# Kernel tuning notes

Hardware: AMD Instinct MI355X
Metric: run time of the kernel (lower is better)

## Reference

```python
import jax, jax.numpy as jnp
import numpy as np


def _conv(x, w, b, pad):
    y = jax.lax.conv_general_dilated(
        x, w, window_strides=(1, 1), padding=[(pad, pad), (pad, pad)],
        dimension_numbers=('NCHW', 'OIHW', 'NCHW'))
    return y + b[None, :, None, None]


def _grid_sample(img, gxn, gyn):
    # img [N,C,H,W]; gxn,gyn [N,H,W] normalized coords.
    # Matches torch grid_sample(mode='bilinear', padding_mode='zeros', align_corners=False).
    N, C, H, W = img.shape
    ix = ((gxn + 1.0) * W - 1.0) * 0.5
    iy = ((gyn + 1.0) * H - 1.0) * 0.5
    ix0 = jnp.floor(ix); iy0 = jnp.floor(iy)
    ix1 = ix0 + 1.0; iy1 = iy0 + 1.0
    wx1 = ix - ix0; wy1 = iy - iy0
    wx0 = 1.0 - wx1; wy0 = 1.0 - wy1
    bidx = jnp.arange(N)[:, None, None]

    def gather(yy, xx):
        valid = (xx >= 0) & (xx < W) & (yy >= 0) & (yy < H)
        xc = jnp.clip(xx, 0, W - 1).astype(jnp.int32)
        yc = jnp.clip(yy, 0, H - 1).astype(jnp.int32)
        v = img[bidx, :, yc, xc]  # [N,H,W,C]
        return jnp.where(valid[..., None], v, jnp.zeros((), img.dtype))

    out = (gather(iy0, ix0) * (wy0 * wx0)[..., None]
           + gather(iy0, ix1) * (wy0 * wx1)[..., None]
           + gather(iy1, ix0) * (wy1 * wx0)[..., None]
           + gather(iy1, ix1) * (wy1 * wx1)[..., None])
    return jnp.transpose(out, (0, 3, 1, 2))  # [N,C,H,W]


def reference(inputs, state, i2h_w, i2h_b, i2f_w, i2f_b, h2f_w, h2f_b,
              flows_w, flows_b, wrap_w, wrap_b):
    B, T, Cin, H, W = inputs.shape
    hid = state.shape[1]
    L = flows_w.shape[0] // 2

    # input-to-hidden for all timesteps at once (as in the torch code)
    i2h = _conv(inputs.reshape(B * T, Cin, H, W), i2h_w, i2h_b, 1)
    i2h = i2h.reshape(B, T, 3 * hid, H, W)
    r_i, u_i, n_i = jnp.split(i2h, 3, axis=2)

    gx, gy = jnp.meshgrid(jnp.arange(W, dtype=inputs.dtype),
                          jnp.arange(H, dtype=inputs.dtype))  # each [H,W]

    def step(h, xs):
        x_t, r_t, u_t, n_t = xs
        f = jnp.tanh(_conv(x_t, i2f_w, i2f_b, 2) + _conv(h, h2f_w, h2f_b, 2))
        flows = _conv(f, flows_w, flows_b, 2).reshape(B, L, 2, H, W)
        # vgrid = grid + (-flow), then normalize by 2*v/size - 1
        vx = gx[None, None] - flows[:, :, 0]
        vy = gy[None, None] - flows[:, :, 1]
        gxn = 2.0 * vx / W - 1.0
        gyn = 2.0 * vy / H - 1.0
        img = jnp.broadcast_to(h[:, None], (B, L, hid, H, W)).reshape(B * L, hid, H, W)
        warped = _grid_sample(img, gxn.reshape(B * L, H, W), gyn.reshape(B * L, H, W))
        warped = warped.reshape(B, L * hid, H, W)
        h2h = _conv(warped, wrap_w, wrap_b, 0)
        r_h, u_h, n_h = jnp.split(h2h, 3, axis=1)
        r = jax.nn.sigmoid(r_t + r_h)
        u = jax.nn.sigmoid(u_t + u_h)
        n = jax.nn.sigmoid(n_t + r * n_h)  # note: sigmoid, faithful to source
        h_new = (1.0 - u) * n + u * h
        return h_new, h_new

    xs = (jnp.swapaxes(inputs, 0, 1),
          jnp.swapaxes(r_i, 0, 1),
          jnp.swapaxes(u_i, 0, 1),
          jnp.swapaxes(n_i, 0, 1))
    h_last, outs = jax.lax.scan(step, state, xs)
    outputs = jnp.swapaxes(outs, 0, 1)  # [B,T,hid,H,W]
    return outputs, h_last


def setup_inputs() -> dict:
    key = jax.random.key(0)
    ks = jax.random.split(key, 8)
    B, T, Cin, H, W = 4, 10, 8, 96, 96
    hid, L = 64, 13

    def w(k, shape):
        fan_in = int(np.prod(shape[1:]))
        return jax.random.normal(k, shape, jnp.float32) * (1.0 / np.sqrt(fan_in))

    return {
        'inputs': jax.random.normal(ks[0], (B, T, Cin, H, W), jnp.float32),
        'state': jnp.zeros((B, hid, H, W), jnp.float32),
        'i2h_w': w(ks[1], (3 * hid, Cin, 3, 3)), 'i2h_b': jnp.zeros((3 * hid,), jnp.float32),
        'i2f_w': w(ks[2], (32, Cin, 5, 5)), 'i2f_b': jnp.zeros((32,), jnp.float32),
        'h2f_w': w(ks[3], (32, hid, 5, 5)), 'h2f_b': jnp.zeros((32,), jnp.float32),
        'flows_w': w(ks[4], (2 * L, 32, 5, 5)), 'flows_b': jnp.zeros((2 * L,), jnp.float32),
        'wrap_w': w(ks[5], (3 * hid, hid * L, 1, 1)), 'wrap_b': jnp.zeros((3 * hid,), jnp.float32),
    }
```

## Files before the change

kernel.cpp:

```cpp
#include <hip/hip_runtime.h>
#include <math.h>

#define HW 9216

typedef __attribute__((ext_vector_type(8))) short short8;
typedef __attribute__((ext_vector_type(4))) short short4v;
typedef __attribute__((ext_vector_type(4))) float float4v;

__device__ __forceinline__ float sigmoidf_(float x) { return 1.0f / (1.0f + expf(-x)); }

__device__ __forceinline__ short bf16rne(float f) {
  unsigned u = __builtin_bit_cast(unsigned, f);
  unsigned r = (u + 0x7FFFu + ((u >> 16) & 1u)) >> 16;
  return (short)r;
}
__device__ __forceinline__ float bf2f(short s) {
  return __builtin_bit_cast(float, ((unsigned)(unsigned short)s) << 16);
}

__global__ __launch_bounds__(256) void k_wconv(const float* __restrict__ w,
                                               short* __restrict__ o)
{
  int i = blockIdx.x * 256 + threadIdx.x;
  if (i >= 192 * 832) return;
  int n = i / 832, k = i % 832;
  int l = k >> 6, c = k & 63;
  o[((size_t)l * 192 + n) * 64 + c] = bf16rne(w[i]);
}

__global__ __launch_bounds__(256) void k_pack(
    const float* __restrict__ wh, const float* __restrict__ wi,
    const float* __restrict__ flw, const float* __restrict__ wih,
    short* __restrict__ whK, short* __restrict__ wiK, short* __restrict__ flK,
    short* __restrict__ i2hK)
{
  int i = blockIdx.x * 256 + threadIdx.x;
  if (i < 51200) {
    int t = i / 2048, rem = i % 2048;
    int o = rem / 64, c = rem % 64;
    whK[i] = bf16rne(wh[((size_t)(o * 64 + c)) * 25 + t]);
  } else if (i < 58368) {
    int j = i - 51200;
    int g = j / 1024, rem = j % 1024;
    int o = rem / 32, k = rem % 32;
    int q = k / 8, ch = k % 8;
    int tap = g * 4 + q;
    wiK[j] = (tap < 25) ? bf16rne(wi[((size_t)(o * 8 + ch)) * 25 + tap]) : (short)0;
  } else if (i < 83968) {
    int j = i - 58368;
    int t = j / 1024, rem = j % 1024;
    int o = rem / 32, c = rem % 32;
    flK[j] = (o < 26) ? bf16rne(flw[((size_t)(o * 32 + c)) * 25 + t]) : (short)0;
  } else {
    int j = i - 83968;
    int g = j / 6144, rem = j % 6144;
    int n = rem / 32, k = rem % 32;
    int q = k / 8, ch = k % 8;
    int tap = g * 4 + q;
    i2hK[j] = (tap < 9) ? bf16rne(wih[((size_t)(n * 8 + ch)) * 9 + tap]) : (short)0;
  }
}

__global__ __launch_bounds__(256) void k_h2bf(const float* __restrict__ st,
                                              short* __restrict__ hbf)
{
  const int tid = threadIdx.x;
  const int pp = tid & 63, cg = tid >> 6;
  const int b = blockIdx.y;
  const int p = blockIdx.x * 64 + pp;
  short s[16];
  #pragma unroll
  for (int k = 0; k < 16; ++k)
    s[k] = bf16rne(st[((size_t)b * 64 + cg * 16 + k) * HW + p]);
  short* dst = hbf + ((size_t)b * HW + p) * 64 + cg * 16;
  *(short8*)dst = *(short8*)&s[0];
  *(short8*)(dst + 8) = *(short8*)&s[8];
}

__global__ __launch_bounds__(256) void k_x2bf(const float* __restrict__ inp,
                                              short* __restrict__ xbf)
{
  const int p  = blockIdx.x * 256 + threadIdx.x;
  const int bt = blockIdx.y;
  short s[8];
  #pragma unroll
  for (int ci = 0; ci < 8; ++ci)
    s[ci] = bf16rne(inp[((size_t)bt * 8 + ci) * HW + p]);
  *(short8*)(xbf + ((size_t)bt * HW + p) * 8) = *(short8*)s;
}

__global__ __launch_bounds__(256) void k_i2h(
    const short* __restrict__ xbf, int t_off,
    const short* __restrict__ wK, const float* __restrict__ bias,
    short* __restrict__ out)
{
  __shared__ __align__(16) short lds_o[192 * 136];
  const int tid  = threadIdx.x;
  const int lane = tid & 63;
  const int w    = tid >> 6;
  const int ml = lane & 15, qd = lane >> 4;
  const int zz = blockIdx.y;
  const int t = (zz >> 2) + t_off, b = zz & 3;
  const int pw0 = blockIdx.x * 128 + w * 32;
  const short* xb = xbf + ((size_t)(b * 10 + t)) * HW * 8;

  short8 afr[2][3];
  #pragma unroll
  for (int s = 0; s < 2; ++s) {
    int px0 = pw0 + s * 16;
    int y0 = px0 / 96, xc0 = px0 % 96;
    #pragma unroll
    for (int g = 0; g < 3; ++g) {
      int tap = g * 4 + qd;
      int dy = tap / 3 - 1;
      int dx = tap % 3 - 1;
      int yy = y0 + dy, xx = xc0 + ml + dx;
      bool v = (tap < 9) && (yy >= 0) && (yy < 96) && (xx >= 0) && (xx < 96);
      short8 a = {};
      if (v) a = *(const short8*)(xb + (size_t)(px0 + ml + dy * 96 + dx) * 8);
      afr[s][g] = a;
    }
  }

  float4v acc[2][12];
  #pragma unroll
  for (int s = 0; s < 2; ++s)
    #pragma unroll
    for (int j = 0; j < 12; ++j)
      #pragma unroll
      for (int r = 0; r < 4; ++r) acc[s][j][r] = 0.0f;

  #pragma unroll
  for (int j = 0; j < 12; ++j) {
    #pragma unroll
    for (int g = 0; g < 3; ++g) {
      short8 bf = *(const short8*)(wK + ((size_t)(g * 192 + j * 16 + ml)) * 32 + qd * 8);
      acc[0][j] = __builtin_amdgcn_mfma_f32_16x16x32_bf16(afr[0][g], bf, acc[0][j], 0, 0, 0);
      acc[1][j] = __builtin_amdgcn_mfma_f32_16x16x32_bf16(afr[1][g], bf, acc[1][j], 0, 0, 0);
    }
  }

  #pragma unroll
  for (int j = 0; j < 12; ++j) {
    float bv = bias[j * 16 + ml];
    #pragma unroll
    for (int s = 0; s < 2; ++s) {
      short4v o4;
      #pragma unroll
      for (int r = 0; r < 4; ++r) o4[r] = bf16rne(acc[s][j][r] + bv);
      *(short4v*)(lds_o + (j * 16 + ml) * 136 + w * 32 + s * 16 + qd * 4) = o4;
    }
  }
  __syncthreads();
  const int pblk = blockIdx.x * 128;
  #pragma unroll
  for (int k = 0; k < 12; ++k) {
    int r = (tid >> 4) + k * 16;
    short8 vvv = *(short8*)(lds_o + r * 136 + (tid & 15) * 8);
    *(short8*)(out + ((size_t)(zz * 192 + r)) * HW + pblk + (tid & 15) * 8) = vvv;
  }
}

__global__ __launch_bounds__(256) void k_f(
    const short* __restrict__ xbf, int t,
    const short* __restrict__ hbf,
    const short* __restrict__ whK,
    const short* __restrict__ wiK,
    const float* __restrict__ bi, const float* __restrict__ bh,
    short* __restrict__ fbf)
{
  const int tid = threadIdx.x;
  const int lane = tid & 63;
  const int w = tid >> 6;
  const int ml = lane & 15, qd = lane >> 4;
  const int b = blockIdx.y;
  const int px0 = blockIdx.x * 64 + w * 16;
  const int y0 = px0 / 96, xc0 = px0 % 96;
  const int xcol = xc0 + ml;
  const int px = px0 + ml;
  const short* hb = hbf + (size_t)b * HW * 64;
  const short* xb = xbf + ((size_t)(b * 10 + t)) * HW * 8;

  float4v acc0 = {0.f, 0.f, 0.f, 0.f};
  float4v acc1 = {0.f, 0.f, 0.f, 0.f};

  #pragma unroll
  for (int ky = 0; ky < 5; ++ky) {
    int yy = y0 + ky - 2;
    if (yy < 0 || yy >= 96) continue;
    #pragma unroll
    for (int kx = 0; kx < 5; ++kx) {
      int xx = xcol + kx - 2;
      bool cv = (xx >= 0) && (xx < 96);
      int off = (ky - 2) * 96 + (kx - 2);
      const short* ap = hb + (size_t)(px + off) * 64 + qd * 8;
      short8 a0 = {}, a1 = {};
      if (cv) { a0 = *(const short8*)ap; a1 = *(const short8*)(ap + 32); }
      int tap = ky * 5 + kx;
      const short* bp = whK + ((size_t)tap * 32 + ml) * 64 + qd * 8;
      short8 b00 = *(const short8*)bp;
      short8 b01 = *(const short8*)(bp + 32);
      short8 b10 = *(const short8*)(bp + 16 * 64);
      short8 b11 = *(const short8*)(bp + 16 * 64 + 32);
      acc0 = __builtin_amdgcn_mfma_f32_16x16x32_bf16(a0, b00, acc0, 0, 0, 0);
      acc0 = __builtin_amdgcn_mfma_f32_16x16x32_bf16(a1, b01, acc0, 0, 0, 0);
      acc1 = __builtin_amdgcn_mfma_f32_16x16x32_bf16(a0, b10, acc1, 0, 0, 0);
      acc1 = __builtin_amdgcn_mfma_f32_16x16x32_bf16(a1, b11, acc1, 0, 0, 0);
    }
  }

  #pragma unroll
  for (int g = 0; g < 7; ++g) {
    int tap = g * 4 + qd;
    int dy = tap / 5 - 2;
    int dx = tap - (dy + 2) * 5 - 2;
    int yy = y0 + dy, xx = xcol + dx;
    bool v = (tap < 25) && (yy >= 0) && (yy < 96) && (xx >= 0) && (xx < 96);
    short8 a = {};
    if (v) a = *(const short8*)(xb + (size_t)(px + dy * 96 + dx) * 8);
    const short* bp = wiK + ((size_t)g * 32 + ml) * 32 + qd * 8;
    short8 b0 = *(const short8*)bp;
    short8 b1 = *(const short8*)(bp + 16 * 32);
    acc0 = __builtin_amdgcn_mfma_f32_16x16x32_bf16(a, b0, acc0, 0, 0, 0);
    acc1 = __builtin_amdgcn_mfma_f32_16x16x32_bf16(a, b1, acc1, 0, 0, 0);
  }

  short* fo = fbf + (size_t)b * HW * 32;
  #pragma unroll
  for (int i = 0; i < 2; ++i) {
    int o = i * 16 + ml;
    float bias = bi[o] + bh[o];
    float4v a = i ? acc1 : acc0;
    #pragma unroll
    for (int r = 0; r < 4; ++r) {
      int p2 = px0 + qd * 4 + r;
      fo[(size_t)p2 * 32 + o] = bf16rne(tanhf(a[r] + bias));
    }
  }
}

__global__ __launch_bounds__(256) void k_flows(
    const short* __restrict__ fbf,
    const short* __restrict__ flK,
    const float* __restrict__ bias,
    float* __restrict__ fls)
{
  const int tid = threadIdx.x;
  const int lane = tid & 63;
  const int w = tid >> 6;
  const int ml = lane & 15, qd = lane >> 4;
  const int b = blockIdx.y;
  const int px0 = blockIdx.x * 64 + w * 16;
  const int y0 = px0 / 96, xc0 = px0 % 96;
  const int xcol = xc0 + ml;
  const int px = px0 + ml;
  const short* fb = fbf + (size_t)b * HW * 32;

  float4v acc0 = {0.f, 0.f, 0.f, 0.f};
  float4v acc1 = {0.f, 0.f, 0.f, 0.f};

  #pragma unroll
  for (int ky = 0; ky < 5; ++ky) {
    int yy = y0 + ky - 2;
    if (yy < 0 || yy >= 96) continue;
    #pragma unroll
    for (int kx = 0; kx < 5; ++kx) {
      int xx = xcol + kx - 2;
      bool cv = (xx >= 0) && (xx < 96);
      int off = (ky - 2) * 96 + (kx - 2);
      short8 a = {};
      if (cv) a = *(const short8*)(fb + (size_t)(px + off) * 32 + qd * 8);
      int tap = ky * 5 + kx;
      const short* bp = flK + ((size_t)tap * 32 + ml) * 32 + qd * 8;
      short8 b0 = *(const short8*)bp;
      short8 b1 = *(const short8*)(bp + 16 * 32);
      acc0 = __builtin_amdgcn_mfma_f32_16x16x32_bf16(a, b0, acc0, 0, 0, 0);
      acc1 = __builtin_amdgcn_mfma_f32_16x16x32_bf16(a, b1, acc1, 0, 0, 0);
    }
  }

  float* fo = fls + (size_t)b * 26 * HW;
  #pragma unroll
  for (int i = 0; i < 2; ++i) {
    int o = i * 16 + ml;
    if (o < 26) {
      float bv = bias[o];
      float4v a = i ? acc1 : acc0;
      #pragma unroll
      for (int r = 0; r < 4; ++r)
        fo[(size_t)o * HW + px0 + qd * 4 + r] = a[r] + bv;
    }
  }
}

__global__ __launch_bounds__(256, 3) void k_fused(
    const float* __restrict__ fls,
    const float* __restrict__ hbase, long long hstr,
    const short* __restrict__ hbf_in,
    const short* __restrict__ i2h,
    const short* __restrict__ wbf,
    const float* __restrict__ wb,
    float* __restrict__ outb, long long ostr,
    short* __restrict__ hbf_out,
    float* __restrict__ lastb)
{
  __shared__ __align__(16) char smem_raw[50176];
  short* lds_v0 = (short*)smem_raw;
  short* lds_v1 = lds_v0 + 64 * 72;
  float* lds_f  = (float*)(smem_raw + 18432);
  float* lds_h  = (float*)smem_raw;
  short* hpack  = (short*)smem_raw;

  const int tid = threadIdx.x;
  const int pp  = tid & 63;
  const int cg  = tid >> 6;
  const int ii  = blockIdx.x;
  const int xcd = ii & 7;
  const int b   = xcd >> 1;
  const int tile = ((ii >> 3) << 1) | (xcd & 1);
  const int p   = tile * 64 + pp;
  const float* hb  = hbase + (size_t)b * hstr;
  const float* flb = fls + (size_t)b * 26 * HW;
  const int ml = pp & 15;
  const int qd = pp >> 4;
  const int px_g = cg * 16 + ml;
  const int p_g  = tile * 64 + px_g;
  const int ypix = p_g / 96, xpix = p_g % 96;
  const short* hvp = hbf_in + ((size_t)b * HW) * 64 + qd * 16;
  const short* wfb = wbf + ((size_t)(48 * cg + ml)) * 64 + qd * 8;

  #pragma unroll
  for (int it = 0; it < 7; ++it) {
    int idx = it * 256 + tid;
    if (idx < 1664) {
      int c = idx >> 6, pp2 = idx & 63;
      lds_f[pp2 * 26 + c] = flb[(size_t)c * HW + tile * 64 + pp2];
    }
  }

  float4v acc[3][4];
  #pragma unroll
  for (int i = 0; i < 3; ++i)
    #pragma unroll
    for (int j = 0; j < 4; ++j)
      #pragma unroll
      for (int r = 0; r < 4; ++r) acc[i][j][r] = 0.0f;

  int   o_[4];
  float wt_[4];
  short8 u_[4][2];
  short8 wp[3][2];
  short vv[16];

  auto comp_offs = [&](int l) {
    float fx = lds_f[px_g * 26 + 2 * l];
    float fy = lds_f[px_g * 26 + 2 * l + 1];
    float ix = (float)xpix - fx - 0.5f;
    float iy = (float)ypix - fy - 0.5f;
    float x0f = floorf(ix), y0f = floorf(iy);
    float wx1 = ix - x0f, wy1 = iy - y0f;
    float wx0 = 1.0f - wx1, wy0 = 1.0f - wy1;
    int x0 = (int)x0f, y0 = (int)y0f;
    bool vx0 = (x0 >= 0) && (x0 < 96);
    bool vx1 = (x0 + 1 >= 0) && (x0 + 1 < 96);
    bool vy0g = (y0 >= 0) && (y0 < 96);
    bool vy1g = (y0 + 1 >= 0) && (y0 + 1 < 96);
    o_[0] = (vx0 && vy0g) ? (y0 * 96 + x0)           : -1;
    o_[1] = (vx1 && vy0g) ? (y0 * 96 + x0 + 1)       : -1;
    o_[2] = (vx0 && vy1g) ? ((y0 + 1) * 96 + x0)     : -1;
    o_[3] = (vx1 && vy1g) ? ((y0 + 1) * 96 + x0 + 1) : -1;
    wt_[0] = wy0 * wx0; wt_[1] = wy0 * wx1; wt_[2] = wy1 * wx0; wt_[3] = wy1 * wx1;
  };
  auto load_gather = [&]() {
    #pragma unroll
    for (int q = 0; q < 4; ++q) {
      short8 z = {};
      u_[q][0] = z; u_[q][1] = z;
      if (o_[q] >= 0) {
        const short* tp = hvp + (size_t)o_[q] * 64;
        u_[q][0] = *(const short8*)tp;
        u_[q][1] = *(const short8*)(tp + 8);
      }
    }
  };
  auto load_w = [&](int l) {
    const short* wsrc = wfb + (size_t)l * 192 * 64;
    #pragma unroll
    for (int i = 0; i < 3; ++i) {
      wp[i][0] = *(const short8*)(wsrc + (i * 16) * 64);
      wp[i][1] = *(const short8*)(wsrc + (i * 16) * 64 + 32);
    }
  };
  auto comp_vv = [&]() {
    float sum[16];
    #pragma unroll
    for (int k = 0; k < 16; ++k) sum[k] = 0.0f;
    #pragma unroll
    for (int q = 0; q < 4; ++q) {
      #pragma unroll
      for (int k = 0; k < 8; ++k) {
        sum[k]     += wt_[q] * bf2f(u_[q][0][k]);
        sum[k + 8] += wt_[q] * bf2f(u_[q][1][k]);
      }
    }
    #pragma unroll
    for (int k = 0; k < 16; ++k) vv[k] = bf16rne(sum[k]);
  };
  auto store_vv = [&](short* buf) {
    *(short8*)(buf + px_g * 72 + qd * 16)     = *(short8*)&vv[0];
    *(short8*)(buf + px_g * 72 + qd * 16 + 8) = *(short8*)&vv[8];
  };

  __syncthreads();
  comp_offs(0);
  load_gather();
  load_w(0);
  comp_vv();
  store_vv(lds_v0);

  for (int l = 0; l < 13; ++l) {
    __syncthreads();
    if (l < 12) {
      comp_offs(l + 1);
      load_gather();
    }
    short* rbuf = (l & 1) ? lds_v1 : lds_v0;
    #pragma unroll
    for (int ks = 0; ks < 2; ++ks) {
      short8 bfr[4];
      #pragma unroll
      for (int j = 0; j < 4; ++j)
        bfr[j] = *(const short8*)(rbuf + (j * 16 + ml) * 72 + ks * 32 + qd * 8);
      #pragma unroll
      for (int i = 0; i < 3; ++i)
        #pragma unroll
        for (int j = 0; j < 4; ++j)
          acc[i][j] = __builtin_amdgcn_mfma_f32_16x16x32_bf16(wp[i][ks], bfr[j], acc[i][j], 0, 0, 0);
    }
    if (l < 12) {
      load_w(l + 1);
      comp_vv();
      store_vv((l & 1) ? lds_v0 : lds_v1);
    }
  }

  __syncthreads();
  #pragma unroll
  for (int i = 0; i < 3; ++i)
    #pragma unroll
    for (int j = 0; j < 4; ++j)
      #pragma unroll
      for (int r = 0; r < 4; ++r) {
        int ch = 48 * cg + i * 16 + qd * 4 + r;
        int px = j * 16 + ml;
        lds_h[ch * 65 + px] = acc[i][j][r];
      }
  __syncthreads();

  const short* i2hb = i2h + (size_t)b * 192 * HW + p;
  float* ob = outb + (size_t)b * ostr;
  float hnv[16];
  #pragma unroll
  for (int k = 0; k < 16; ++k) {
    int cch = cg + k * 4;
    float rh = lds_h[cch * 65 + pp] + wb[cch];
    float uh = lds_h[(64 + cch) * 65 + pp] + wb[64 + cch];
    float nh = lds_h[(128 + cch) * 65 + pp] + wb[128 + cch];
    float rt = bf2f(i2hb[(size_t)cch * HW]);
    float ut = bf2f(i2hb[(size_t)(64 + cch) * HW]);
    float nt = bf2f(i2hb[(size_t)(128 + cch) * HW]);
    float rr = sigmoidf_(rt + rh);
    float uu = sigmoidf_(ut + uh);
    float nn = sigmoidf_(nt + rr * nh);
    float hp = hb[(size_t)cch * HW + p];
    float hn = (1.0f - uu) * nn + uu * hp;
    ob[(size_t)cch * HW + p] = hn;
    if (lastb) lastb[((size_t)b * 64 + cch) * HW + p] = hn;
    hnv[k] = hn;
  }

  __syncthreads();
  #pragma unroll
  for (int k = 0; k < 16; ++k)
    hpack[pp * 80 + cg + 4 * k] = bf16rne(hnv[k]);
  __syncthreads();
  {
    int px = tid >> 2, g = tid & 3;
    short8 a0 = *(short8*)(hpack + px * 80 + g * 16);
    short8 a1 = *(short8*)(hpack + px * 80 + g * 16 + 8);
    short* dst = hbf_out + ((size_t)b * HW + tile * 64 + px) * 64 + g * 16;
    *(short8*)dst = a0;
    *(short8*)(dst + 8) = a1;
  }
}

extern "C" void kernel_launch(void* const* d_in, const int* in_sizes, int n_in,
                              void* d_out, int out_size, void* d_ws, size_t ws_size,
                              hipStream_t stream)
{
  const float* inp   = (const float*)d_in[0];
  const float* state = (const float*)d_in[1];
  const float* i2h_w = (const float*)d_in[2];
  const float* i2h_b = (const float*)d_in[3];
  const float* i2f_w = (const float*)d_in[4];
  const float* i2f_b = (const float*)d_in[5];
  const float* h2f_w = (const float*)d_in[6];
  const float* h2f_b = (const float*)d_in[7];
  const float* fl_w  = (const float*)d_in[8];
  const float* fl_b  = (const float*)d_in[9];
  const float* wr_w  = (const float*)d_in[10];
  const float* wr_b  = (const float*)d_in[11];
  float* out = (float*)d_out;
  float* ws  = (float*)d_ws;

  const long long F_I2HB1 = 3538944;
  const long long F_FBF   = 589824;
  const long long F_FLS   = 958464;
  const long long F_HB    = 1179648;
  const long long F_XBF   = 1474560;
  const long long F_WBF   = 79872;
  const long long F_WHK   = 25600;
  const long long F_WIK   = 3584;
  const long long F_FLK   = 12800;
  const long long F_I2HK  = 9216;
  const long long OB      = (long long)10 * 64 * HW;

  const long long fixed = F_FBF + F_FLS + 2 * F_HB + F_XBF + F_WBF
                        + F_WHK + F_WIK + F_FLK + F_I2HK;
  bool batched = ws_size >= (size_t)(10 * F_I2HB1 + fixed) * 4ULL;
  long long i2h_fl = batched ? 10 * F_I2HB1 : F_I2HB1;

  short* ws_i2h = (short*)ws;
  float* fwp    = ws + i2h_fl;
  float* ws_fbf_f = fwp;              fwp += F_FBF;
  float* ws_fls   = fwp;              fwp += F_FLS;
  float* hbfA_f   = fwp;              fwp += F_HB;
  float* hbfB_f   = fwp;              fwp += F_HB;
  float* xbf_f    = fwp;              fwp += F_XBF;
  float* wbf_f    = fwp;              fwp += F_WBF;
  float* whK_f    = fwp;              fwp += F_WHK;
  float* wiK_f    = fwp;              fwp += F_WIK;
  float* flK_f    = fwp;              fwp += F_FLK;
  float* i2hK_f   = fwp;
  short* ws_fbf  = (short*)ws_fbf_f;
  short* hbfA    = (short*)hbfA_f;
  short* hbfB    = (short*)hbfB_f;
  short* ws_xbf  = (short*)xbf_f;
  short* ws_wbf  = (short*)wbf_f;
  short* ws_whK  = (short*)whK_f;
  short* ws_wiK  = (short*)wiK_f;
  short* ws_flK  = (short*)flK_f;
  short* ws_i2hK = (short*)i2hK_f;

  k_wconv<<<dim3(624), 256, 0, stream>>>(wr_w, ws_wbf);
  k_pack<<<dim3(400), 256, 0, stream>>>(h2f_w, i2f_w, fl_w, i2h_w,
                                        ws_whK, ws_wiK, ws_flK, ws_i2hK);
  k_h2bf<<<dim3(144, 4), 256, 0, stream>>>(state, hbfA);
  k_x2bf<<<dim3(36, 40), 256, 0, stream>>>(inp, ws_xbf);
  if (batched)
    k_i2h<<<dim3(72, 40), 256, 0, stream>>>(ws_xbf, 0, ws_i2hK, i2h_b, ws_i2h);

  for (int t = 0; t < 10; ++t) {
    const float* hbase = (t == 0) ? state : (out + (size_t)(t - 1) * 64 * HW);
    long long hstr = (t == 0) ? (long long)64 * HW : OB;
    short* hin  = (t & 1) ? hbfB : hbfA;
    short* hout = (t & 1) ? hbfA : hbfB;

    if (!batched)
      k_i2h<<<dim3(72, 4), 256, 0, stream>>>(ws_xbf, t, ws_i2hK, i2h_b, ws_i2h);
    k_f<<<dim3(144, 4), 256, 0, stream>>>(ws_xbf, t, hin, ws_whK, ws_wiK,
                                          i2f_b, h2f_b, ws_fbf);
    k_flows<<<dim3(144, 4), 256, 0, stream>>>(ws_fbf, ws_flK, fl_b, ws_fls);

    const short* i2h_t = batched ? (ws_i2h + (size_t)t * 2 * F_I2HB1) : ws_i2h;
    float* outbase = out + (size_t)t * 64 * HW;
    float* lastb = (t == 9) ? (out + (size_t)4 * 10 * 64 * HW) : nullptr;
    k_fused<<<dim3(576), 256, 0, stream>>>(ws_fls, hbase, hstr, hin, i2h_t,
                                           ws_wbf, wr_b, outbase, OB, hout, lastb);
  }
}
```

Before: 1.612 ms.

## Give each wave its own pixel slice to drop per-layer barriers in wrap MFMA

Changes the MFMA work split in the fused warp/wrap kernel. Before, each wave computed 48 output channels across all 64 pixels, which needed a shared double-buffered LDS tile and a barrier every flow layer. Now each wave computes all 192 channels for its own 16 pixels, which it gathers itself, so the per-layer __syncthreads and the second LDS buffer go away. In exchange, each wave loads the full weight slice from global/L2 every layer (4x more weight traffic), and the weight loads are no longer prefetched a layer ahead.

```diff
diff --git a/kernel.cpp b/kernel.cpp
--- a/kernel.cpp
+++ b/kernel.cpp
@@ -305,11 +305,10 @@
     float* __restrict__ lastb)
 {
   __shared__ __align__(16) char smem_raw[50176];
-  short* lds_v0 = (short*)smem_raw;
-  short* lds_v1 = lds_v0 + 64 * 72;
-  float* lds_f  = (float*)(smem_raw + 18432);
-  float* lds_h  = (float*)smem_raw;
-  short* hpack  = (short*)smem_raw;
+  short* lds_v = (short*)smem_raw;
+  float* lds_f = (float*)(smem_raw + 9216);
+  float* lds_h = (float*)smem_raw;
+  short* hpack = (short*)smem_raw;
 
   const int tid = threadIdx.x;
   const int pp  = tid & 63;
@@ -323,11 +322,10 @@
   const float* flb = fls + (size_t)b * 26 * HW;
   const int ml = pp & 15;
   const int qd = pp >> 4;
-  const int px_g = cg * 16 + ml;
-  const int p_g  = tile * 64 + px_g;
+  const int px_w = cg * 16 + ml;
+  const int p_g  = tile * 64 + px_w;
   const int ypix = p_g / 96, xpix = p_g % 96;
   const short* hvp = hbf_in + ((size_t)b * HW) * 64 + qd * 16;
-  const short* wfb = wbf + ((size_t)(48 * cg + ml)) * 64 + qd * 8;
 
   #pragma unroll
   for (int it = 0; it < 7; ++it) {
@@ -338,23 +336,20 @@
     }
   }
 
-  float4v acc[3][4];
-  #pragma unroll
-  for (int i = 0; i < 3; ++i)
-    #pragma unroll
-    for (int j = 0; j < 4; ++j)
-      #pragma unroll
-      for (int r = 0; r < 4; ++r) acc[i][j][r] = 0.0f;
+  float4v acc[12];
+  #pragma unroll
+  for (int i = 0; i < 12; ++i)
+    #pragma unroll
+    for (int r = 0; r < 4; ++r) acc[i][r] = 0.0f;
 
   int   o_[4];
   float wt_[4];
   short8 u_[4][2];
-  short8 wp[3][2];
   short vv[16];
 
   auto comp_offs = [&](int l) {
-    float fx = lds_f[px_g * 26 + 2 * l];
-    float fy = lds_f[px_g * 26 + 2 * l + 1];
+    float fx = lds_f[px_w * 26 + 2 * l];
+    float fy = lds_f[px_w * 26 + 2 * l + 1];
     float ix = (float)xpix - fx - 0.5f;
     float iy = (float)ypix - fy - 0.5f;
     float x0f = floorf(ix), y0f = floorf(iy);
@@ -383,14 +378,6 @@
       }
     }
   };
-  auto load_w = [&](int l) {
-    const short* wsrc = wfb + (size_t)l * 192 * 64;
-    #pragma unroll
-    for (int i = 0; i < 3; ++i) {
-      wp[i][0] = *(const short8*)(wsrc + (i * 16) * 64);
-      wp[i][1] = *(const short8*)(wsrc + (i * 16) * 64 + 32);
-    }
-  };
   auto comp_vv = [&]() {
     float sum[16];
     #pragma unroll
@@ -406,55 +393,44 @@
     #pragma unroll
     for (int k = 0; k < 16; ++k) vv[k] = bf16rne(sum[k]);
   };
-  auto store_vv = [&](short* buf) {
-    *(short8*)(buf + px_g * 72 + qd * 16)     = *(short8*)&vv[0];
-    *(short8*)(buf + px_g * 72 + qd * 16 + 8) = *(short8*)&vv[8];
+  auto store_vv = [&]() {
+    *(short8*)(lds_v + px_w * 72 + qd * 16)     = *(short8*)&vv[0];
+    *(short8*)(lds_v + px_w * 72 + qd * 16 + 8) = *(short8*)&vv[8];
   };
 
   __syncthreads();
   comp_offs(0);
   load_gather();
-  load_w(0);
   comp_vv();
-  store_vv(lds_v0);
+  store_vv();
 
   for (int l = 0; l < 13; ++l) {
-    __syncthreads();
     if (l < 12) {
       comp_offs(l + 1);
       load_gather();
     }
-    short* rbuf = (l & 1) ? lds_v1 : lds_v0;
-    #pragma unroll
-    for (int ks = 0; ks < 2; ++ks) {
-      short8 bfr[4];
-      #pragma unroll
-      for (int j = 0; j < 4; ++j)
-        bfr[j] = *(const short8*)(rbuf + (j * 16 + ml) * 72 + ks * 32 + qd * 8);
-      #pragma unroll
-      for (int i = 0; i < 3; ++i)
-        #pragma unroll
-        for (int j = 0; j < 4; ++j)
-          acc[i][j] = __builtin_amdgcn_mfma_f32_16x16x32_bf16(wp[i][ks], bfr[j], acc[i][j], 0, 0, 0);
+    short8 bfr0 = *(const short8*)(lds_v + px_w * 72 + qd * 8);
+    short8 bfr1 = *(const short8*)(lds_v + px_w * 72 + 32 + qd * 8);
+    const short* wsrc = wbf + (size_t)l * 192 * 64;
+    #pragma unroll
+    for (int i = 0; i < 12; ++i) {
+      short8 a0 = *(const short8*)(wsrc + (size_t)(i * 16 + ml) * 64 + qd * 8);
+      short8 a1 = *(const short8*)(wsrc + (size_t)(i * 16 + ml) * 64 + 32 + qd * 8);
+      acc[i] = __builtin_amdgcn_mfma_f32_16x16x32_bf16(a0, bfr0, acc[i], 0, 0, 0);
+      acc[i] = __builtin_amdgcn_mfma_f32_16x16x32_bf16(a1, bfr1, acc[i], 0, 0, 0);
     }
     if (l < 12) {
-      load_w(l + 1);
       comp_vv();
-      store_vv((l & 1) ? lds_v0 : lds_v1);
+      store_vv();
     }
   }
 
   __syncthreads();
   #pragma unroll
-  for (int i = 0; i < 3; ++i)
-    #pragma unroll
-    for (int j = 0; j < 4; ++j)
-      #pragma unroll
-      for (int r = 0; r < 4; ++r) {
-        int ch = 48 * cg + i * 16 + qd * 4 + r;
-        int px = j * 16 + ml;
-        lds_h[ch * 65 + px] = acc[i][j][r];
-      }
+  for (int i = 0; i < 12; ++i)
+    #pragma unroll
+    for (int r = 0; r < 4; ++r)
+      lds_h[(i * 16 + qd * 4 + r) * 65 + cg * 16 + ml] = acc[i][r];
   __syncthreads();
 
   const short* i2hb = i2h + (size_t)b * 192 * HW + p;
```

Measured after the change: 2.376 ms. 47.4% more time.
